# Kernel tuning notes

Measured on AMD Instinct MI355X. Metric: run time of the kernel, lower is better.

## Reference

```python
import jax, jax.numpy as jnp
import numpy as np

WS = 8      # window size
SS = 4      # shift size
NH = 4      # num heads
EPS = 1e-5
MLP_RATIO = 4


def _win_part(x, ws):
    # x: [B,D,H,W,C] -> [B*nD*nH*nW, ws^3, C]
    B, D, H, W, C = x.shape
    x = x.reshape(B, D // ws, ws, H // ws, ws, W // ws, ws, C)
    x = x.transpose(0, 1, 3, 5, 2, 4, 6, 7)
    return x.reshape(-1, ws * ws * ws, C)


def _win_rev(w, ws, B, D, H, W):
    C = w.shape[-1]
    x = w.reshape(B, D // ws, H // ws, W // ws, ws, ws, ws, C)
    x = x.transpose(0, 1, 4, 2, 5, 3, 6, 7)
    return x.reshape(B, D, H, W, C)


def _ln(x, g, b):
    m = jnp.mean(x, axis=-1, keepdims=True)
    v = jnp.mean((x - m) ** 2, axis=-1, keepdims=True)
    return (x - m) / jnp.sqrt(v + EPS) * g + b


def _rel_index(ws):
    coords = np.stack(np.meshgrid(np.arange(ws), np.arange(ws), np.arange(ws), indexing='ij'))  # [3,ws,ws,ws]
    cf = coords.reshape(3, -1)                      # [3, ws^3]
    rel = (cf[:, :, None] - cf[:, None, :]).transpose(1, 2, 0) + (ws - 1)  # [N,N,3]
    return rel[..., 0] * (2 * ws - 1) ** 2 + rel[..., 1] * (2 * ws - 1) + rel[..., 2]


def _attn_mask(D, H, W, ws, ss):
    img = np.zeros((1, D, H, W, 1), dtype=np.float32)
    cnt = 0
    sl = (slice(0, -ws), slice(-ws, -ss), slice(-ss, None))
    for d in sl:
        for h in sl:
            for w in sl:
                img[:, d, h, w, :] = cnt
                cnt += 1
    mw = np.asarray(_win_part(jnp.asarray(img), ws))[..., 0]  # [nW, ws^3]
    diff = mw[:, None, :] - mw[:, :, None]
    return np.where(diff != 0, -100.0, 0.0).astype(np.float32)


def setup_inputs() -> dict:
    key = jax.random.key(0)
    ks = jax.random.split(key, 12)
    B, D, H, W, C = 1, 16, 64, 64, 128
    mh = MLP_RATIO * C
    s = 0.02
    return {
        'x': jax.random.normal(ks[0], (B, D, H, W, C), jnp.float32),
        'attn_mask': jnp.asarray(_attn_mask(D, H, W, WS, SS)),
        'rel_index': jnp.asarray(_rel_index(WS), jnp.int32),
        'rel_bias': jax.random.normal(ks[1], ((2 * WS - 1) ** 3, NH), jnp.float32) * s,
        'qkv_w': jax.random.normal(ks[2], (3 * C, C), jnp.float32) * s,
        'qkv_b': jnp.zeros((3 * C,), jnp.float32),
        'proj_w': jax.random.normal(ks[3], (C, C), jnp.float32) * s,
        'proj_b': jnp.zeros((C,), jnp.float32),
        'norm1_g': jnp.ones((C,), jnp.float32),
        'norm1_b': jnp.zeros((C,), jnp.float32),
        'norm2_g': jnp.ones((C,), jnp.float32),
        'norm2_b': jnp.zeros((C,), jnp.float32),
        'mlp_w1': jax.random.normal(ks[4], (mh, C), jnp.float32) * s,
        'mlp_b1': jnp.zeros((mh,), jnp.float32),
        'mlp_w2': jax.random.normal(ks[5], (C, mh), jnp.float32) * s,
        'mlp_b2': jnp.zeros((C,), jnp.float32),
    }


def reference(x, attn_mask, rel_index, rel_bias, qkv_w, qkv_b, proj_w, proj_b,
              norm1_g, norm1_b, norm2_g, norm2_b, mlp_w1, mlp_b1, mlp_w2, mlp_b2):
    B, D, H, W, C = x.shape
    ws, ss, nh = WS, SS, NH
    hd = C // nh
    scale = hd ** -0.5
    N = ws ** 3
    shortcut = x
    h = _ln(x, norm1_g, norm1_b)
    h = jnp.roll(h, (-ss, -ss, -ss), axis=(1, 2, 3))
    xw = _win_part(h, ws)                 # [B_, N, C]
    B_ = xw.shape[0]
    nW = attn_mask.shape[0]
    qkv = xw @ qkv_w.T + qkv_b            # [B_, N, 3C]
    qkv = qkv.reshape(B_, N, 3, nh, hd).transpose(2, 0, 3, 1, 4)  # [3,B_,h,N,hd]
    q, k, v = qkv[0] * scale, qkv[1], qkv[2]
    attn = jnp.einsum('bhnd,bhmd->bhnm', q, k)
    rpe = rel_bias[rel_index.reshape(-1)].reshape(N, N, nh).transpose(2, 0, 1)  # [h,N,N]
    attn = attn + rpe[None]
    attn = attn.reshape(B_ // nW, nW, nh, N, N) + attn_mask[None, :, None]
    attn = jax.nn.softmax(attn.reshape(B_, nh, N, N), axis=-1)
    out = jnp.einsum('bhnm,bhmd->bhnd', attn, v).transpose(0, 2, 1, 3).reshape(B_, N, C)
    out = out @ proj_w.T + proj_b
    out = _win_rev(out, ws, B, D, H, W)
    out = jnp.roll(out, (ss, ss, ss), axis=(1, 2, 3))
    x = shortcut + out
    h2 = _ln(x, norm2_g, norm2_b)
    h2 = jax.nn.gelu(h2 @ mlp_w1.T + mlp_b1, approximate=False)
    return x + h2 @ mlp_w2.T + mlp_b2
```

## Files before the change

### kernel.cpp

```cpp
#include <hip/hip_runtime.h>
#include <math.h>

typedef __bf16 bf16;
typedef __bf16 bf16x8 __attribute__((ext_vector_type(8)));
typedef float f32x4 __attribute__((ext_vector_type(4)));
typedef unsigned short u16;

#define LDA 136

__global__ void sniff_k(const unsigned* __restrict__ xw_, int* __restrict__ flag) {
  if (threadIdx.x == 0 && blockIdx.x == 0) {
    int cnt = 0;
    for (int i = 0; i < 256; i++) {
      unsigned e = (xw_[i] >> 7) & 0xFFu;
      cnt += (e >= 100u && e <= 140u) ? 1 : 0;
    }
    *flag = (cnt >= 150) ? 1 : 0;
  }
}

__global__ __launch_bounds__(256) void canon_big_k(const void* __restrict__ src,
                                                   bf16* __restrict__ dst,
                                                   const int* __restrict__ flag) {
  int i = (blockIdx.x * 256 + threadIdx.x) * 8;
  if (*flag) {
    *(bf16x8*)&dst[i] = *(const bf16x8*)((const bf16*)src + i);
  } else {
    const float* s = (const float*)src + i;
    bf16x8 v;
#pragma unroll
    for (int j = 0; j < 8; j++) v[j] = (bf16)s[j];
    *(bf16x8*)&dst[i] = v;
  }
}

struct CanonArgs {
  const void* src[13];
  bf16* dst[13];
  int n[13];
};

__global__ __launch_bounds__(256) void canon_small_k(CanonArgs a,
                                                     const int* __restrict__ flag) {
  int ti = blockIdx.y;
  int i = blockIdx.x * 256 + threadIdx.x;
  if (i >= a.n[ti]) return;
  if (*flag)
    a.dst[ti][i] = ((const bf16*)a.src[ti])[i];
  else
    a.dst[ti][i] = (bf16)((const float*)a.src[ti])[i];
}

__global__ __launch_bounds__(256) void rpe_k(const int* __restrict__ ridx,
                                             const bf16* __restrict__ rbias,
                                             bf16* __restrict__ rpe) {
  int t = blockIdx.x * 256 + threadIdx.x;
  int h = t >> 18, nm = t & 262143;
  rpe[t] = rbias[ridx[nm] * 4 + h];
}

template <int ROLL>
__global__ __launch_bounds__(256) void ln_k(const bf16* __restrict__ x,
                                            const bf16* __restrict__ g,
                                            const bf16* __restrict__ bsh,
                                            bf16* __restrict__ out) {
  int wave = threadIdx.x >> 6, lane = threadIdx.x & 63;
  int tok = blockIdx.x * 4 + wave;
  size_t src;
  if (ROLL) {
    int win = tok >> 9, pos = tok & 511;
    int rd = (win >> 6) * 8 + (pos >> 6);
    int rh = ((win >> 3) & 7) * 8 + ((pos >> 3) & 7);
    int rw = (win & 7) * 8 + (pos & 7);
    int od = (rd + 4) & 15, oh = (rh + 4) & 63, ow = (rw + 4) & 63;
    src = (size_t)((od * 64 + oh) * 64 + ow) * 128;
  } else {
    src = (size_t)tok * 128;
  }
  int ch = lane * 2;
  float f0 = (float)x[src + ch], f1 = (float)x[src + ch + 1];
  float s = f0 + f1, sq = f0 * f0 + f1 * f1;
#pragma unroll
  for (int d = 1; d < 64; d <<= 1) {
    s += __shfl_xor(s, d);
    sq += __shfl_xor(sq, d);
  }
  float mean = s * (1.f / 128.f);
  float var = sq * (1.f / 128.f) - mean * mean;
  float rstd = rsqrtf(fmaxf(var, 0.f) + 1e-5f);
  float o0 = (f0 - mean) * rstd * (float)g[ch] + (float)bsh[ch];
  float o1 = (f1 - mean) * rstd * (float)g[ch + 1] + (float)bsh[ch + 1];
  out[(size_t)tok * 128 + ch] = (bf16)o0;
  out[(size_t)tok * 128 + ch + 1] = (bf16)o1;
}

template <int EPI, int N_, int K_>
__global__ __launch_bounds__(256) void gemm_k(const bf16* __restrict__ A,
                                              const bf16* __restrict__ B,
                                              const bf16* __restrict__ bias,
                                              void* __restrict__ outv,
                                              const bf16* __restrict__ resid,
                                              const int* __restrict__ flag) {
  __shared__ __align__(16) u16 As[64 * LDA];
  __shared__ __align__(16) u16 Bs[64 * LDA];
  const int t = threadIdx.x;
  const int wave = t >> 6, lane = t & 63, l15 = lane & 15, quad = lane >> 4;
  const int m0 = blockIdx.x * 64, n0 = blockIdx.y * 64;
  int fl = 0;
  if constexpr (EPI == 3) fl = *flag;
  f32x4 acc[4] = {};
  for (int kc = 0; kc < K_; kc += 128) {
    __syncthreads();
#pragma unroll
    for (int i = 0; i < 4; i++) {
      int id = t + i * 256;
      int row = id >> 4, c = (id & 15) * 8;
      *(bf16x8*)&As[row * LDA + c] =
          *(const bf16x8*)(A + (size_t)(m0 + row) * K_ + kc + c);
      *(bf16x8*)&Bs[row * LDA + c] =
          *(const bf16x8*)(B + (size_t)(n0 + row) * K_ + kc + c);
    }
    __syncthreads();
#pragma unroll
    for (int ks = 0; ks < 4; ks++) {
      bf16x8 a = *(const bf16x8*)&As[(wave * 16 + l15) * LDA + ks * 32 + quad * 8];
#pragma unroll
      for (int nt = 0; nt < 4; nt++) {
        bf16x8 b = *(const bf16x8*)&Bs[(nt * 16 + l15) * LDA + ks * 32 + quad * 8];
        acc[nt] = __builtin_amdgcn_mfma_f32_16x16x32_bf16(a, b, acc[nt], 0, 0, 0);
      }
    }
  }
  const float qscale = 0.17677669529663687f;
#pragma unroll
  for (int r = 0; r < 4; r++) {
    int tok = m0 + wave * 16 + quad * 4 + r;
    size_t obase;
    if constexpr (EPI == 1) {
      int win = tok >> 9, pos = tok & 511;
      int rd = (win >> 6) * 8 + (pos >> 6);
      int rh = ((win >> 3) & 7) * 8 + ((pos >> 3) & 7);
      int rw = (win & 7) * 8 + (pos & 7);
      int od = (rd + 4) & 15, oh = (rh + 4) & 63, ow = (rw + 4) & 63;
      obase = (size_t)((od * 64 + oh) * 64 + ow) * 128;
    } else {
      obase = (size_t)tok * N_;
    }
#pragma unroll
    for (int nt = 0; nt < 4; nt++) {
      int gn = n0 + nt * 16 + l15;
      float v = acc[nt][r] + (float)bias[gn];
      if constexpr (EPI == 0) {
        if (gn < 128) v *= qscale;
      }
      if constexpr (EPI == 2) {
        v = 0.5f * v * (1.f + erff(v * 0.70710678118654752f));
      }
      if constexpr (EPI == 1) {
        v += (float)resid[obase + gn];
      }
      if constexpr (EPI == 3) {
        v += (float)resid[obase + gn];
        if (fl)
          ((bf16*)outv)[obase + gn] = (bf16)v;
        else
          ((float*)outv)[obase + gn] = v;
      } else {
        ((bf16*)outv)[obase + gn] = (bf16)v;
      }
    }
  }
}

__global__ __launch_bounds__(256) void attn_k(const bf16* __restrict__ qkv,
                                              const bf16* __restrict__ rpe,
                                              bf16* __restrict__ att) {
  __shared__ __align__(16) u16 sVt[32 * 72];
  __shared__ __align__(16) u16 sP[4][32 * 72];
  __shared__ unsigned char lbl[512];
  const int t = threadIdx.x;
  const int b = blockIdx.x;
  const int win = b >> 4, head = (b >> 2) & 3, qc = b & 3;
  const int wave = t >> 6, lane = t & 63, l15 = lane & 15, quad = lane >> 4;

  {
    int wd = win >> 6, wh = (win >> 3) & 7, wwi = win & 7;
    for (int p = t; p < 512; p += 256) {
      int gd = wd * 8 + (p >> 6), gh = wh * 8 + ((p >> 3) & 7),
          gw = wwi * 8 + (p & 7);
      int ld = gd < 8 ? 0 : (gd < 12 ? 1 : 2);
      int lh = gh < 56 ? 0 : (gh < 60 ? 1 : 2);
      int lw = gw < 56 ? 0 : (gw < 60 ? 1 : 2);
      lbl[p] = (unsigned char)((ld << 4) | (lh << 2) | lw);
    }
  }
  __syncthreads();

  const size_t wbase = (size_t)win * 512 * 384;
  const int qbase = qc * 128 + wave * 32;
  bf16x8 qa[2];
#pragma unroll
  for (int mt = 0; mt < 2; mt++)
    qa[mt] = *(const bf16x8*)(qkv + wbase +
                              (size_t)(qbase + mt * 16 + l15) * 384 + head * 32 +
                              quad * 8);
  f32x4 O[2][2] = {};
  float ms[2][4], ls[2][4];
#pragma unroll
  for (int mt = 0; mt < 2; mt++)
#pragma unroll
    for (int r = 0; r < 4; r++) {
      ms[mt][r] = -1e30f;
      ls[mt][r] = 0.f;
    }
  const bf16* rpeh = rpe + (size_t)head * 512 * 512;
  const f32x4 zf = {0.f, 0.f, 0.f, 0.f};

  for (int kt = 0; kt < 8; kt++) {
    __syncthreads();
    {
      int row = t >> 2, c4 = t & 3;
      bf16x8 vv = *(const bf16x8*)(qkv + wbase + (size_t)(kt * 64 + row) * 384 +
                                   256 + head * 32 + c4 * 8);
#pragma unroll
      for (int j = 0; j < 8; j++)
        sVt[(c4 * 8 + j) * 72 + row] = __builtin_bit_cast(u16, vv[j]);
    }
    __syncthreads();

    f32x4 S[2][4];
#pragma unroll
    for (int nt = 0; nt < 4; nt++) {
      bf16x8 kb = *(const bf16x8*)(qkv + wbase +
                                   (size_t)(kt * 64 + nt * 16 + l15) * 384 + 128 +
                                   head * 32 + quad * 8);
      S[0][nt] = __builtin_amdgcn_mfma_f32_16x16x32_bf16(qa[0], kb, zf, 0, 0, 0);
      S[1][nt] = __builtin_amdgcn_mfma_f32_16x16x32_bf16(qa[1], kb, zf, 0, 0, 0);
    }
#pragma unroll
    for (int nt = 0; nt < 4; nt++) {
      int kcol = kt * 64 + nt * 16 + l15;
      int lk = lbl[kcol];
#pragma unroll
      for (int mt = 0; mt < 2; mt++)
#pragma unroll
        for (int r = 0; r < 4; r++) {
          int q = qbase + mt * 16 + quad * 4 + r;
          float bv = (float)rpeh[(size_t)q * 512 + kcol];
          if (lbl[q] != lk) bv -= 100.f;
          S[mt][nt][r] += bv;
        }
    }
#pragma unroll
    for (int mt = 0; mt < 2; mt++)
#pragma unroll
      for (int r = 0; r < 4; r++) {
        float mx = fmaxf(fmaxf(S[mt][0][r], S[mt][1][r]),
                         fmaxf(S[mt][2][r], S[mt][3][r]));
        mx = fmaxf(mx, __shfl_xor(mx, 1));
        mx = fmaxf(mx, __shfl_xor(mx, 2));
        mx = fmaxf(mx, __shfl_xor(mx, 4));
        mx = fmaxf(mx, __shfl_xor(mx, 8));
        float mnew = fmaxf(ms[mt][r], mx);
        float alpha = __expf(fminf(ms[mt][r] - mnew, 0.f));
        ms[mt][r] = mnew;
        float rs = 0.f;
#pragma unroll
        for (int nt = 0; nt < 4; nt++) {
          float p = __expf(fminf(S[mt][nt][r] - mnew, 0.f));
          S[mt][nt][r] = p;
          rs += p;
        }
        rs += __shfl_xor(rs, 1);
        rs += __shfl_xor(rs, 2);
        rs += __shfl_xor(rs, 4);
        rs += __shfl_xor(rs, 8);
        ls[mt][r] = ls[mt][r] * alpha + rs;
        O[mt][0][r] *= alpha;
        O[mt][1][r] *= alpha;
      }
    u16* pw = sP[wave];
#pragma unroll
    for (int mt = 0; mt < 2; mt++)
#pragma unroll
      for (int nt = 0; nt < 4; nt++)
#pragma unroll
        for (int r = 0; r < 4; r++)
          pw[(mt * 16 + quad * 4 + r) * 72 + nt * 16 + l15] =
              __builtin_bit_cast(u16, (bf16)S[mt][nt][r]);
#pragma unroll
    for (int s = 0; s < 2; s++) {
      bf16x8 pa0 = *(const bf16x8*)&pw[l15 * 72 + s * 32 + quad * 8];
      bf16x8 pa1 = *(const bf16x8*)&pw[(16 + l15) * 72 + s * 32 + quad * 8];
      bf16x8 vb0 = *(const bf16x8*)&sVt[l15 * 72 + s * 32 + quad * 8];
      bf16x8 vb1 = *(const bf16x8*)&sVt[(16 + l15) * 72 + s * 32 + quad * 8];
      O[0][0] = __builtin_amdgcn_mfma_f32_16x16x32_bf16(pa0, vb0, O[0][0], 0, 0, 0);
      O[0][1] = __builtin_amdgcn_mfma_f32_16x16x32_bf16(pa0, vb1, O[0][1], 0, 0, 0);
      O[1][0] = __builtin_amdgcn_mfma_f32_16x16x32_bf16(pa1, vb0, O[1][0], 0, 0, 0);
      O[1][1] = __builtin_amdgcn_mfma_f32_16x16x32_bf16(pa1, vb1, O[1][1], 0, 0, 0);
    }
  }
#pragma unroll
  for (int mt = 0; mt < 2; mt++)
#pragma unroll
    for (int nd = 0; nd < 2; nd++)
#pragma unroll
      for (int r = 0; r < 4; r++) {
        int q = qbase + mt * 16 + quad * 4 + r;
        att[((size_t)win * 512 + q) * 128 + head * 32 + nd * 16 + l15] =
            (bf16)(O[mt][nd][r] / ls[mt][r]);
      }
}

extern "C" void kernel_launch(void* const* d_in, const int* in_sizes, int n_in,
                              void* d_out, int out_size, void* d_ws,
                              size_t ws_size, hipStream_t stream) {
  const int* rel_index = (const int*)d_in[2];
  char* w = (char*)d_ws;

  int* flag = (int*)w;
  bf16* rb_c = (bf16*)(w + (64ull << 10));
  bf16* qw_c = (bf16*)(w + (128ull << 10));
  bf16* pw_c = (bf16*)(w + (256ull << 10));
  bf16* w1_c = (bf16*)(w + (320ull << 10));
  bf16* w2_c = (bf16*)(w + (512ull << 10));
  bf16* qb_c = (bf16*)(w + (704ull << 10));
  bf16* pb_c = (bf16*)(w + (708ull << 10));
  bf16* g1_c = (bf16*)(w + (712ull << 10));
  bf16* b1n_c = (bf16*)(w + (716ull << 10));
  bf16* g2_c = (bf16*)(w + (720ull << 10));
  bf16* b2n_c = (bf16*)(w + (724ull << 10));
  bf16* mb1_c = (bf16*)(w + (728ull << 10));
  bf16* mb2_c = (bf16*)(w + (732ull << 10));
  bf16* x_c = (bf16*)(w + (1ull << 20));
  bf16* xw = (bf16*)(w + (17ull << 20));
  bf16* qkvb = (bf16*)(w + (33ull << 20));
  bf16* rpe = (bf16*)(w + (97ull << 20));
  bf16* x2 = (bf16*)(w + (99ull << 20));
  bf16* att = xw;
  bf16* h2 = xw;
  bf16* a1 = qkvb;

  sniff_k<<<1, 64, 0, stream>>>((const unsigned*)d_in[0], flag);
  canon_big_k<<<4096, 256, 0, stream>>>(d_in[0], x_c, flag);

  CanonArgs ca;
  const int srcidx[13] = {3, 4, 5, 6, 7, 8, 9, 10, 11, 12, 13, 14, 15};
  bf16* dsts[13] = {rb_c, qw_c, qb_c, pw_c, pb_c, g1_c, b1n_c,
                    g2_c, b2n_c, w1_c, mb1_c, w2_c, mb2_c};
  for (int i = 0; i < 13; i++) {
    ca.src[i] = d_in[srcidx[i]];
    ca.dst[i] = dsts[i];
    ca.n[i] = in_sizes[srcidx[i]];
  }
  canon_small_k<<<dim3(256, 13), 256, 0, stream>>>(ca, flag);

  rpe_k<<<4096, 256, 0, stream>>>(rel_index, rb_c, rpe);
  ln_k<1><<<16384, 256, 0, stream>>>(x_c, g1_c, b1n_c, xw);
  gemm_k<0, 384, 128><<<dim3(1024, 6), 256, 0, stream>>>(xw, qw_c, qb_c, qkvb,
                                                         nullptr, flag);
  attn_k<<<2048, 256, 0, stream>>>(qkvb, rpe, att);
  gemm_k<1, 128, 128><<<dim3(1024, 2), 256, 0, stream>>>(att, pw_c, pb_c, x2,
                                                         x_c, flag);
  ln_k<0><<<16384, 256, 0, stream>>>(x2, g2_c, b2n_c, h2);
  gemm_k<2, 512, 128><<<dim3(1024, 8), 256, 0, stream>>>(h2, w1_c, mb1_c, a1,
                                                         nullptr, flag);
  gemm_k<3, 128, 512><<<dim3(1024, 2), 256, 0, stream>>>(a1, w2_c, mb2_c, d_out,
                                                         x2, flag);
}
```

Before: 449.1 us.

## Enlarge GEMM tiles, head-major QKV layout, transposed RPE staged in LDS

GEMM tiles grow from 64x64 to 128x128 with a 2x2 wave layout, 64-wide K steps and register prefetch before the LDS store, which raises reuse per loaded element. The QKV GEMM now writes Q/K/V in a [tensor][head][window][pos][d] layout so attention reads contiguous per-head rows. The relative position bias is precomputed transposed and tiles of it are staged through LDS for coalesced loads, and attention blocks are reordered so neighbouring windows share bias tiles in cache. LayerNorm uses paired vector loads and stores. An extra barrier is added in attention, and the larger tiles mean fewer blocks in flight.

```diff
diff --git a/kernel.cpp b/kernel.cpp
--- a/kernel.cpp
+++ b/kernel.cpp
@@ -5,8 +5,12 @@
 typedef __bf16 bf16x8 __attribute__((ext_vector_type(8)));
 typedef float f32x4 __attribute__((ext_vector_type(4)));
 typedef unsigned short u16;
-
-#define LDA 136
+typedef u16 u16x2 __attribute__((ext_vector_type(2)));
+typedef u16 u16x4 __attribute__((ext_vector_type(4)));
+
+__device__ __forceinline__ float b2f(u16 b) {
+  return (float)__builtin_bit_cast(bf16, b);
+}
 
 __global__ void sniff_k(const unsigned* __restrict__ xw_, int* __restrict__ flag) {
   if (threadIdx.x == 0 && blockIdx.x == 0) {
@@ -53,10 +57,10 @@
 
 __global__ __launch_bounds__(256) void rpe_k(const int* __restrict__ ridx,
                                              const bf16* __restrict__ rbias,
-                                             bf16* __restrict__ rpe) {
+                                             bf16* __restrict__ rpeT) {
   int t = blockIdx.x * 256 + threadIdx.x;
-  int h = t >> 18, nm = t & 262143;
-  rpe[t] = rbias[ridx[nm] * 4 + h];
+  int q = t & 511, m = (t >> 9) & 511, h = t >> 18;
+  rpeT[t] = rbias[ridx[q * 512 + m] * 4 + h];
 }
 
 template <int ROLL>
@@ -78,7 +82,8 @@
     src = (size_t)tok * 128;
   }
   int ch = lane * 2;
-  float f0 = (float)x[src + ch], f1 = (float)x[src + ch + 1];
+  u16x2 xv = *(const u16x2*)(x + src + ch);
+  float f0 = b2f(xv[0]), f1 = b2f(xv[1]);
   float s = f0 + f1, sq = f0 * f0 + f1 * f1;
 #pragma unroll
   for (int d = 1; d < 64; d <<= 1) {
@@ -88,10 +93,11 @@
   float mean = s * (1.f / 128.f);
   float var = sq * (1.f / 128.f) - mean * mean;
   float rstd = rsqrtf(fmaxf(var, 0.f) + 1e-5f);
-  float o0 = (f0 - mean) * rstd * (float)g[ch] + (float)bsh[ch];
-  float o1 = (f1 - mean) * rstd * (float)g[ch + 1] + (float)bsh[ch + 1];
-  out[(size_t)tok * 128 + ch] = (bf16)o0;
-  out[(size_t)tok * 128 + ch + 1] = (bf16)o1;
+  u16x2 gv = *(const u16x2*)(g + ch), bv = *(const u16x2*)(bsh + ch);
+  u16x2 ov;
+  ov[0] = __builtin_bit_cast(u16, (bf16)((f0 - mean) * rstd * b2f(gv[0]) + b2f(bv[0])));
+  ov[1] = __builtin_bit_cast(u16, (bf16)((f1 - mean) * rstd * b2f(gv[1]) + b2f(bv[1])));
+  *(u16x2*)(out + (size_t)tok * 128 + ch) = ov;
 }
 
 template <int EPI, int N_, int K_>
@@ -101,109 +107,137 @@
                                               void* __restrict__ outv,
                                               const bf16* __restrict__ resid,
                                               const int* __restrict__ flag) {
-  __shared__ __align__(16) u16 As[64 * LDA];
-  __shared__ __align__(16) u16 Bs[64 * LDA];
+  __shared__ __align__(16) u16 As[128 * 72];
+  __shared__ __align__(16) u16 Bs[128 * 72];
   const int t = threadIdx.x;
   const int wave = t >> 6, lane = t & 63, l15 = lane & 15, quad = lane >> 4;
-  const int m0 = blockIdx.x * 64, n0 = blockIdx.y * 64;
+  const int m0 = blockIdx.x * 128, n0 = blockIdx.y * 128;
   int fl = 0;
   if constexpr (EPI == 3) fl = *flag;
-  f32x4 acc[4] = {};
-  for (int kc = 0; kc < K_; kc += 128) {
+  f32x4 acc[4][4] = {};
+  const int wr = (wave >> 1) * 64, wc = (wave & 1) * 64;
+  const int srow = t >> 3, scol = (t & 7) * 8;
+  for (int kc = 0; kc < K_; kc += 64) {
+    bf16x8 av[4], bv[4];
+#pragma unroll
+    for (int p = 0; p < 4; p++) {
+      int row = p * 32 + srow;
+      av[p] = *(const bf16x8*)(A + (size_t)(m0 + row) * K_ + kc + scol);
+      bv[p] = *(const bf16x8*)(B + (size_t)(n0 + row) * K_ + kc + scol);
+    }
     __syncthreads();
 #pragma unroll
-    for (int i = 0; i < 4; i++) {
-      int id = t + i * 256;
-      int row = id >> 4, c = (id & 15) * 8;
-      *(bf16x8*)&As[row * LDA + c] =
-          *(const bf16x8*)(A + (size_t)(m0 + row) * K_ + kc + c);
-      *(bf16x8*)&Bs[row * LDA + c] =
-          *(const bf16x8*)(B + (size_t)(n0 + row) * K_ + kc + c);
+    for (int p = 0; p < 4; p++) {
+      int row = p * 32 + srow;
+      *(bf16x8*)&As[row * 72 + scol] = av[p];
+      *(bf16x8*)&Bs[row * 72 + scol] = bv[p];
     }
     __syncthreads();
 #pragma unroll
-    for (int ks = 0; ks < 4; ks++) {
-      bf16x8 a = *(const bf16x8*)&As[(wave * 16 + l15) * LDA + ks * 32 + quad * 8];
-#pragma unroll
-      for (int nt = 0; nt < 4; nt++) {
-        bf16x8 b = *(const bf16x8*)&Bs[(nt * 16 + l15) * LDA + ks * 32 + quad * 8];
-        acc[nt] = __builtin_amdgcn_mfma_f32_16x16x32_bf16(a, b, acc[nt], 0, 0, 0);
-      }
+    for (int ks = 0; ks < 2; ks++) {
+      bf16x8 a[4], b[4];
+#pragma unroll
+      for (int i = 0; i < 4; i++) {
+        a[i] = *(const bf16x8*)&As[(wr + i * 16 + l15) * 72 + ks * 32 + quad * 8];
+        b[i] = *(const bf16x8*)&Bs[(wc + i * 16 + l15) * 72 + ks * 32 + quad * 8];
+      }
+#pragma unroll
+      for (int i = 0; i < 4; i++)
+#pragma unroll
+        for (int j = 0; j < 4; j++)
+          acc[i][j] =
+              __builtin_amdgcn_mfma_f32_16x16x32_bf16(a[i], b[j], acc[i][j], 0, 0, 0);
     }
   }
   const float qscale = 0.17677669529663687f;
 #pragma unroll
-  for (int r = 0; r < 4; r++) {
-    int tok = m0 + wave * 16 + quad * 4 + r;
-    size_t obase;
-    if constexpr (EPI == 1) {
-      int win = tok >> 9, pos = tok & 511;
-      int rd = (win >> 6) * 8 + (pos >> 6);
-      int rh = ((win >> 3) & 7) * 8 + ((pos >> 3) & 7);
-      int rw = (win & 7) * 8 + (pos & 7);
-      int od = (rd + 4) & 15, oh = (rh + 4) & 63, ow = (rw + 4) & 63;
-      obase = (size_t)((od * 64 + oh) * 64 + ow) * 128;
-    } else {
-      obase = (size_t)tok * N_;
-    }
-#pragma unroll
-    for (int nt = 0; nt < 4; nt++) {
-      int gn = n0 + nt * 16 + l15;
-      float v = acc[nt][r] + (float)bias[gn];
-      if constexpr (EPI == 0) {
-        if (gn < 128) v *= qscale;
-      }
-      if constexpr (EPI == 2) {
-        v = 0.5f * v * (1.f + erff(v * 0.70710678118654752f));
-      }
+  for (int i = 0; i < 4; i++) {
+#pragma unroll
+    for (int r = 0; r < 4; r++) {
+      int tok = m0 + wr + i * 16 + quad * 4 + r;
+      size_t obase = 0;
       if constexpr (EPI == 1) {
-        v += (float)resid[obase + gn];
-      }
-      if constexpr (EPI == 3) {
-        v += (float)resid[obase + gn];
-        if (fl)
+        int win = tok >> 9, pos = tok & 511;
+        int rd = (win >> 6) * 8 + (pos >> 6);
+        int rh = ((win >> 3) & 7) * 8 + ((pos >> 3) & 7);
+        int rw = (win & 7) * 8 + (pos & 7);
+        int od = (rd + 4) & 15, oh = (rh + 4) & 63, ow = (rw + 4) & 63;
+        obase = (size_t)((od * 64 + oh) * 64 + ow) * 128;
+      } else if constexpr (EPI != 0) {
+        obase = (size_t)tok * N_;
+      }
+#pragma unroll
+      for (int j = 0; j < 4; j++) {
+        int gn = n0 + wc + j * 16 + l15;
+        float v = acc[i][j][r] + (float)bias[gn];
+        if constexpr (EPI == 0) {
+          int tensor = gn >> 7, c = gn & 127, head = c >> 5, d = c & 31;
+          if (tensor == 0) v *= qscale;
+          int win = tok >> 9, pos = tok & 511;
+          size_t off = ((((size_t)tensor * 4 + head) * 128 + win) * 512 + pos) * 32 + d;
+          ((bf16*)outv)[off] = (bf16)v;
+        } else if constexpr (EPI == 1) {
+          v += (float)resid[obase + gn];
           ((bf16*)outv)[obase + gn] = (bf16)v;
-        else
-          ((float*)outv)[obase + gn] = v;
-      } else {
-        ((bf16*)outv)[obase + gn] = (bf16)v;
+        } else if constexpr (EPI == 2) {
+          v = 0.5f * v * (1.f + erff(v * 0.70710678118654752f));
+          ((bf16*)outv)[obase + gn] = (bf16)v;
+        } else {
+          v += (float)resid[obase + gn];
+          if (fl)
+            ((bf16*)outv)[obase + gn] = (bf16)v;
+          else
+            ((float*)outv)[obase + gn] = v;
+        }
       }
     }
   }
 }
 
 __global__ __launch_bounds__(256) void attn_k(const bf16* __restrict__ qkv,
-                                              const bf16* __restrict__ rpe,
+                                              const bf16* __restrict__ rpeT,
                                               bf16* __restrict__ att) {
   __shared__ __align__(16) u16 sVt[32 * 72];
   __shared__ __align__(16) u16 sP[4][32 * 72];
+  __shared__ __align__(16) u16 sR[64 * 136];
   __shared__ unsigned char lbl[512];
   const int t = threadIdx.x;
-  const int b = blockIdx.x;
-  const int win = b >> 4, head = (b >> 2) & 3, qc = b & 3;
+  const int p = blockIdx.x;
+  const int win = ((p >> 7) << 3) | (p & 7);
+  const int j = (p >> 3) & 15;
+  const int head = j >> 2, qc = j & 3;
   const int wave = t >> 6, lane = t & 63, l15 = lane & 15, quad = lane >> 4;
 
   {
     int wd = win >> 6, wh = (win >> 3) & 7, wwi = win & 7;
-    for (int p = t; p < 512; p += 256) {
-      int gd = wd * 8 + (p >> 6), gh = wh * 8 + ((p >> 3) & 7),
-          gw = wwi * 8 + (p & 7);
+    for (int pp = t; pp < 512; pp += 256) {
+      int gd = wd * 8 + (pp >> 6), gh = wh * 8 + ((pp >> 3) & 7),
+          gw = wwi * 8 + (pp & 7);
       int ld = gd < 8 ? 0 : (gd < 12 ? 1 : 2);
       int lh = gh < 56 ? 0 : (gh < 60 ? 1 : 2);
       int lw = gw < 56 ? 0 : (gw < 60 ? 1 : 2);
-      lbl[p] = (unsigned char)((ld << 4) | (lh << 2) | lw);
+      lbl[pp] = (unsigned char)((ld << 4) | (lh << 2) | lw);
     }
   }
   __syncthreads();
 
-  const size_t wbase = (size_t)win * 512 * 384;
+  const size_t hw32 = (size_t)512 * 32;
+  const bf16* qp = qkv + ((size_t)(0 * 4 + head) * 128 + win) * hw32;
+  const bf16* kp = qkv + ((size_t)(1 * 4 + head) * 128 + win) * hw32;
+  const bf16* vp = qkv + ((size_t)(2 * 4 + head) * 128 + win) * hw32;
   const int qbase = qc * 128 + wave * 32;
+
+  int lq[2][4];
+#pragma unroll
+  for (int mt = 0; mt < 2; mt++)
+#pragma unroll
+    for (int r = 0; r < 4; r++) lq[mt][r] = lbl[qbase + mt * 16 + quad * 4 + r];
+
   bf16x8 qa[2];
 #pragma unroll
   for (int mt = 0; mt < 2; mt++)
-    qa[mt] = *(const bf16x8*)(qkv + wbase +
-                              (size_t)(qbase + mt * 16 + l15) * 384 + head * 32 +
-                              quad * 8);
+    qa[mt] = *(const bf16x8*)(qp + (size_t)(qbase + mt * 16 + l15) * 32 + quad * 8);
+
   f32x4 O[2][2] = {};
   float ms[2][4], ls[2][4];
 #pragma unroll
@@ -213,43 +247,51 @@
       ms[mt][r] = -1e30f;
       ls[mt][r] = 0.f;
     }
-  const bf16* rpeh = rpe + (size_t)head * 512 * 512;
   const f32x4 zf = {0.f, 0.f, 0.f, 0.f};
+  const bf16* rpeh = rpeT + (size_t)head * 512 * 512;
 
   for (int kt = 0; kt < 8; kt++) {
     __syncthreads();
     {
       int row = t >> 2, c4 = t & 3;
-      bf16x8 vv = *(const bf16x8*)(qkv + wbase + (size_t)(kt * 64 + row) * 384 +
-                                   256 + head * 32 + c4 * 8);
-#pragma unroll
-      for (int j = 0; j < 8; j++)
-        sVt[(c4 * 8 + j) * 72 + row] = __builtin_bit_cast(u16, vv[j]);
+      bf16x8 vv = *(const bf16x8*)(vp + (size_t)(kt * 64 + row) * 32 + c4 * 8);
+#pragma unroll
+      for (int jj = 0; jj < 8; jj++)
+        sVt[(c4 * 8 + jj) * 72 + row] = __builtin_bit_cast(u16, vv[jj]);
+    }
+    {
+      int rr = t >> 4, cc = (t & 15) * 8;
+#pragma unroll
+      for (int pp = 0; pp < 4; pp++) {
+        int row = pp * 16 + rr;
+        bf16x8 rv = *(const bf16x8*)(rpeh + (size_t)(kt * 64 + row) * 512 +
+                                     qc * 128 + cc);
+        *(bf16x8*)&sR[row * 136 + cc] = rv;
+      }
     }
     __syncthreads();
 
     f32x4 S[2][4];
 #pragma unroll
     for (int nt = 0; nt < 4; nt++) {
-      bf16x8 kb = *(const bf16x8*)(qkv + wbase +
-                                   (size_t)(kt * 64 + nt * 16 + l15) * 384 + 128 +
-                                   head * 32 + quad * 8);
+      bf16x8 kb =
+          *(const bf16x8*)(kp + (size_t)(kt * 64 + nt * 16 + l15) * 32 + quad * 8);
       S[0][nt] = __builtin_amdgcn_mfma_f32_16x16x32_bf16(qa[0], kb, zf, 0, 0, 0);
       S[1][nt] = __builtin_amdgcn_mfma_f32_16x16x32_bf16(qa[1], kb, zf, 0, 0, 0);
     }
 #pragma unroll
     for (int nt = 0; nt < 4; nt++) {
-      int kcol = kt * 64 + nt * 16 + l15;
-      int lk = lbl[kcol];
-#pragma unroll
-      for (int mt = 0; mt < 2; mt++)
+      int lk = lbl[kt * 64 + nt * 16 + l15];
+#pragma unroll
+      for (int mt = 0; mt < 2; mt++) {
+        u16x4 rv = *(const u16x4*)&sR[(nt * 16 + l15) * 136 + mt * 16 + quad * 4];
 #pragma unroll
         for (int r = 0; r < 4; r++) {
-          int q = qbase + mt * 16 + quad * 4 + r;
-          float bv = (float)rpeh[(size_t)q * 512 + kcol];
-          if (lbl[q] != lk) bv -= 100.f;
+          float bv = b2f(rv[r]);
+          if (lq[mt][r] != lk) bv -= 100.f;
           S[mt][nt][r] += bv;
         }
+      }
     }
 #pragma unroll
     for (int mt = 0; mt < 2; mt++)
@@ -267,9 +309,9 @@
         float rs = 0.f;
 #pragma unroll
         for (int nt = 0; nt < 4; nt++) {
-          float p = __expf(fminf(S[mt][nt][r] - mnew, 0.f));
-          S[mt][nt][r] = p;
-          rs += p;
+          float pe = __expf(fminf(S[mt][nt][r] - mnew, 0.f));
+          S[mt][nt][r] = pe;
+          rs += pe;
         }
         rs += __shfl_xor(rs, 1);
         rs += __shfl_xor(rs, 2);
@@ -288,6 +330,7 @@
         for (int r = 0; r < 4; r++)
           pw[(mt * 16 + quad * 4 + r) * 72 + nt * 16 + l15] =
               __builtin_bit_cast(u16, (bf16)S[mt][nt][r]);
+    __syncthreads();
 #pragma unroll
     for (int s = 0; s < 2; s++) {
       bf16x8 pa0 = *(const bf16x8*)&pw[l15 * 72 + s * 32 + quad * 8];
@@ -335,7 +378,7 @@
   bf16* x_c = (bf16*)(w + (1ull << 20));
   bf16* xw = (bf16*)(w + (17ull << 20));
   bf16* qkvb = (bf16*)(w + (33ull << 20));
-  bf16* rpe = (bf16*)(w + (97ull << 20));
+  bf16* rpeT = (bf16*)(w + (97ull << 20));
   bf16* x2 = (bf16*)(w + (99ull << 20));
   bf16* att = xw;
   bf16* h2 = xw;
@@ -355,16 +398,16 @@
   }
   canon_small_k<<<dim3(256, 13), 256, 0, stream>>>(ca, flag);
 
-  rpe_k<<<4096, 256, 0, stream>>>(rel_index, rb_c, rpe);
+  rpe_k<<<4096, 256, 0, stream>>>(rel_index, rb_c, rpeT);
   ln_k<1><<<16384, 256, 0, stream>>>(x_c, g1_c, b1n_c, xw);
-  gemm_k<0, 384, 128><<<dim3(1024, 6), 256, 0, stream>>>(xw, qw_c, qb_c, qkvb,
-                                                         nullptr, flag);
-  attn_k<<<2048, 256, 0, stream>>>(qkvb, rpe, att);
-  gemm_k<1, 128, 128><<<dim3(1024, 2), 256, 0, stream>>>(att, pw_c, pb_c, x2,
-                                                         x_c, flag);
+  gemm_k<0, 384, 128><<<dim3(512, 3), 256, 0, stream>>>(xw, qw_c, qb_c, qkvb,
+                                                        nullptr, flag);
+  attn_k<<<2048, 256, 0, stream>>>(qkvb, rpeT, att);
+  gemm_k<1, 128, 128><<<dim3(512, 1), 256, 0, stream>>>(att, pw_c, pb_c, x2,
+                                                        x_c, flag);
   ln_k<0><<<16384, 256, 0, stream>>>(x2, g2_c, b2n_c, h2);
-  gemm_k<2, 512, 128><<<dim3(1024, 8), 256, 0, stream>>>(h2, w1_c, mb1_c, a1,
-                                                         nullptr, flag);
-  gemm_k<3, 128, 512><<<dim3(1024, 2), 256, 0, stream>>>(a1, w2_c, mb2_c, d_out,
-                                                         x2, flag);
-}
+  gemm_k<2, 512, 128><<<dim3(512, 4), 256, 0, stream>>>(h2, w1_c, mb1_c, a1,
+                                                        nullptr, flag);
+  gemm_k<3, 128, 512><<<dim3(512, 1), 256, 0, stream>>>(a1, w2_c, mb2_c, d_out,
+                                                        x2, flag);
+}
```

New measurement: 454.2 us. Within noise of the previous version (+1.1%).
